# Kernel optimization log

Measured on AMD Instinct MI355X. Metric: run time of the kernel, lower is better.

The kernel has to match this reference:

```python
import jax, jax.numpy as jnp
import numpy as np

EOS = 1e-10
ALPHA = 0.5
TEMPERATURE = 1.0
BIAS = 0.0001
N_NODES = 8192
N_EDGES = 262144
INPUT_DIM = 512
HIDDEN = 128


def setup_inputs() -> dict:
    key = jax.random.key(0)
    ks = jax.random.split(key, 7)
    features = jax.random.normal(ks[0], (N_NODES, INPUT_DIM), dtype=jnp.float32)
    W_emb = jax.random.normal(ks[1], (HIDDEN, INPUT_DIM), dtype=jnp.float32) * (1.0 / np.sqrt(INPUT_DIM))
    b_emb = jax.random.normal(ks[2], (HIDDEN,), dtype=jnp.float32) * 0.01
    W_edge = jax.random.normal(ks[3], (1, 2 * HIDDEN), dtype=jnp.float32) * (1.0 / np.sqrt(2 * HIDDEN))
    b_edge = jax.random.normal(ks[4], (1,), dtype=jnp.float32) * 0.01
    noise = jax.random.uniform(ks[5], (N_EDGES,), dtype=jnp.float32)
    edges = jax.random.randint(ks[6], (2, N_EDGES), 0, N_NODES, dtype=jnp.int64 if jax.config.jax_enable_x64 else jnp.int32)
    return {"features": features, "W_emb": W_emb, "b_emb": b_emb,
            "W_edge": W_edge, "b_edge": b_edge, "noise": noise, "edges": edges}


def _sym_normalize(adj):
    # inv_sqrt_degree[:,None] * adj * inv_sqrt_degree[None,:]
    inv_sqrt_deg = 1.0 / (jnp.sqrt(adj.sum(axis=1)) + EOS)
    return adj * inv_sqrt_deg[:, None] * inv_sqrt_deg[None, :]


def reference(features, W_emb, b_emb, W_edge, b_edge, noise, edges):
    n = N_NODES
    # node embedding: single Linear + ReLU
    h = jax.nn.relu(features @ W_emb.T + b_emb)            # [N, H]
    e0, e1 = edges[0], edges[1]
    h0, h1 = h[e0], h[e1]                                   # [E, H] gathers
    Wa, Wb = W_edge[0, :HIDDEN], W_edge[0, HIDDEN:]
    s1 = h0 @ Wa + h1 @ Wb + b_edge[0]                       # edge_mlp(cat(h0,h1))
    s2 = h1 @ Wa + h0 @ Wb + b_edge[0]                       # edge_mlp(cat(h1,h0))
    raw = 0.5 * (s1 + s2)                                    # [E]
    # gumbel gate: eps = (bias-(1-bias))*rand + (1-bias)
    eps = (BIAS - (1.0 - BIAS)) * noise + (1.0 - BIAS)
    gate = (jnp.log(eps) - jnp.log1p(-eps) + raw) / TEMPERATURE
    weights_lp = jax.nn.sigmoid(gate)                        # [E]
    weights_hp = 1.0 - weights_lp
    eye = jnp.eye(n, dtype=features.dtype)
    # scatter edge weights to dense adjacency (assignment semantics, like torch adj[e0,e1]=w)
    adj_lp = jnp.zeros((n, n), dtype=features.dtype).at[e0, e1].set(weights_lp) + eye
    adj_lp = _sym_normalize(adj_lp)
    adj_hp = jnp.zeros((n, n), dtype=features.dtype).at[e0, e1].set(weights_hp) + eye
    adj_hp = _sym_normalize(adj_hp)
    mask = jnp.zeros((n, n), dtype=features.dtype).at[e0, e1].set(1.0)
    adj_hp = eye - adj_hp * mask * ALPHA
    return (adj_lp, adj_hp, weights_lp, weights_hp)
```

## Files before the change

### kernel.cpp

```cpp
#include <hip/hip_runtime.h>
#include <cstdint>
#include <cstddef>

#define N_NODES 8192
#define N_EDGES 262144
#define INPUT_DIM 512
#define HIDDEN 128
#define ALPHA 0.5f
#define EOS 1e-10f

#define BK 32
#define BM 32

__global__ __launch_bounds__(512) void k1_g(
    const float* __restrict__ F, const float* __restrict__ W,
    const float* __restrict__ bemb, const float* __restrict__ Wedge,
    float* __restrict__ g)
{
    __shared__ float Fl[BK][BM];
    __shared__ float Wl[BK][HIDDEN];
    int tid = threadIdx.x;
    int tx = tid & 15;
    int ty = tid >> 4;
    int node0 = blockIdx.x * BM;

    float acc[8];
#pragma unroll
    for (int j = 0; j < 8; j++) acc[j] = 0.f;

    for (int d0 = 0; d0 < INPUT_DIM; d0 += BK) {
        if (tid < 256) {
            int r = tid >> 3, dd = (tid & 7) << 2;
            float4 v = *(const float4*)&F[(size_t)(node0 + r) * INPUT_DIM + d0 + dd];
            Fl[dd + 0][r] = v.x; Fl[dd + 1][r] = v.y;
            Fl[dd + 2][r] = v.z; Fl[dd + 3][r] = v.w;
        }
#pragma unroll
        for (int i = 0; i < 2; i++) {
            int idx = tid + i * 512;
            int kr = idx >> 3, dd = (idx & 7) << 2;
            float4 v = *(const float4*)&W[(size_t)kr * INPUT_DIM + d0 + dd];
            Wl[dd + 0][kr] = v.x; Wl[dd + 1][kr] = v.y;
            Wl[dd + 2][kr] = v.z; Wl[dd + 3][kr] = v.w;
        }
        __syncthreads();
#pragma unroll
        for (int kk = 0; kk < BK; kk++) {
            float f0 = Fl[kk][ty];
            float4 wA = *(float4*)&Wl[kk][tx * 8];
            float4 wB = *(float4*)&Wl[kk][tx * 8 + 4];
            acc[0] = fmaf(f0, wA.x, acc[0]);
            acc[1] = fmaf(f0, wA.y, acc[1]);
            acc[2] = fmaf(f0, wA.z, acc[2]);
            acc[3] = fmaf(f0, wA.w, acc[3]);
            acc[4] = fmaf(f0, wB.x, acc[4]);
            acc[5] = fmaf(f0, wB.y, acc[5]);
            acc[6] = fmaf(f0, wB.z, acc[6]);
            acc[7] = fmaf(f0, wB.w, acc[7]);
        }
        __syncthreads();
    }
    float s = 0.f;
#pragma unroll
    for (int j = 0; j < 8; j++) {
        int k = tx * 8 + j;
        float h = acc[j] + bemb[k];
        h = h > 0.f ? h : 0.f;
        s += h * (Wedge[k] + Wedge[HIDDEN + k]);
    }
#pragma unroll
    for (int off = 8; off > 0; off >>= 1)
        s += __shfl_down(s, off, 16);
    if (tx == 0) g[node0 + ty] = s;
}

__global__ __launch_bounds__(256) void k2_edges(
    const int* __restrict__ edges, const float* __restrict__ noise,
    const float* __restrict__ g, const float* __restrict__ bedge,
    float* __restrict__ wlp, float* __restrict__ whp, int* __restrict__ lp_int)
{
    int i = blockIdx.x * 256 + threadIdx.x;
    if (i >= N_EDGES) return;
    int e0 = edges[i], e1 = edges[N_EDGES + i];
    float raw = 0.5f * (g[e0] + g[e1]) + bedge[0];
    const float c1 = (float)(0.0001 - (1.0 - 0.0001));
    const float c2 = (float)(1.0 - 0.0001);
    float eps = c1 * noise[i] + c2;
    float gate = logf(eps) - log1pf(-eps) + raw;
    float w = 1.f / (1.f + expf(-gate));
    wlp[i] = w;
    whp[i] = 1.f - w;
    atomicMax(&lp_int[(size_t)e0 * N_NODES + e1], i + 1);
}

__global__ __launch_bounds__(256) void k3_winner(
    const int* __restrict__ edges, const int* __restrict__ lp_int,
    const float* __restrict__ wlp, const float* __restrict__ whp,
    unsigned char* __restrict__ flags,
    float* __restrict__ deg_lp, float* __restrict__ deg_hp)
{
    int i = blockIdx.x * 256 + threadIdx.x;
    if (i >= N_EDGES) return;
    int e0 = edges[i], e1 = edges[N_EDGES + i];
    bool win = (lp_int[(size_t)e0 * N_NODES + e1] == i + 1);
    flags[i] = win ? 1 : 0;
    if (win) {
        atomicAdd(&deg_lp[e0], wlp[i]);
        atomicAdd(&deg_hp[e0], whp[i]);
    }
}

__global__ __launch_bounds__(256) void k4_inv(
    const float* __restrict__ deg_lp, const float* __restrict__ deg_hp,
    float* __restrict__ inv_lp, float* __restrict__ inv_hp)
{
    int r = blockIdx.x * 256 + threadIdx.x;
    if (r >= N_NODES) return;
    inv_lp[r] = 1.f / (sqrtf(deg_lp[r] + 1.f) + EOS);
    inv_hp[r] = 1.f / (sqrtf(deg_hp[r] + 1.f) + EOS);
}

__global__ __launch_bounds__(256) void k5_bg(
    float* __restrict__ LP, float* __restrict__ HP,
    const float* __restrict__ inv_lp)
{
    size_t idx = (size_t)blockIdx.x * 256 + threadIdx.x;
    int row = (int)(idx >> 11);
    int c4 = (int)(idx & 2047) << 2;
    float4 lp = make_float4(0.f, 0.f, 0.f, 0.f);
    float4 hp = make_float4(0.f, 0.f, 0.f, 0.f);
    int d = row - c4;
    if (d >= 0 && d < 4) {
        float il = inv_lp[row];
        ((float*)&lp)[d] = il * il;
        ((float*)&hp)[d] = 1.0f;
    }
    *(float4*)&LP[idx << 2] = lp;
    *(float4*)&HP[idx << 2] = hp;
}

__global__ __launch_bounds__(256) void k6_fix(
    const int* __restrict__ edges, const unsigned char* __restrict__ flags,
    const float* __restrict__ wlp, const float* __restrict__ whp,
    const float* __restrict__ inv_lp, const float* __restrict__ inv_hp,
    float* __restrict__ LP, float* __restrict__ HP)
{
    int i = blockIdx.x * 256 + threadIdx.x;
    if (i >= N_EDGES) return;
    if (!flags[i]) return;
    int r = edges[i], c = edges[N_EDGES + i];
    size_t cell = (size_t)r * N_NODES + c;
    float diag = (r == c) ? 1.f : 0.f;
    LP[cell] = (wlp[i] + diag) * inv_lp[r] * inv_lp[c];
    HP[cell] = diag - (whp[i] + diag) * inv_hp[r] * inv_hp[c] * ALPHA;
}

extern "C" void kernel_launch(void* const* d_in, const int* in_sizes, int n_in,
                              void* d_out, int out_size, void* d_ws, size_t ws_size,
                              hipStream_t stream) {
    const float* F     = (const float*)d_in[0];
    const float* W     = (const float*)d_in[1];
    const float* bemb  = (const float*)d_in[2];
    const float* Wedge = (const float*)d_in[3];
    const float* bedge = (const float*)d_in[4];
    const float* noise = (const float*)d_in[5];
    const int*   edges = (const int*)d_in[6];

    float* out = (float*)d_out;
    float* LP  = out;
    float* HP  = out + (size_t)N_NODES * N_NODES;
    float* wlp = HP + (size_t)N_NODES * N_NODES;
    float* whp = wlp + N_EDGES;

    char* ws = (char*)d_ws;
    float* g       = (float*)(ws);
    float* deg_lp  = (float*)(ws + 32768);
    float* deg_hp  = (float*)(ws + 65536);
    float* inv_lp  = (float*)(ws + 98304);
    float* inv_hp  = (float*)(ws + 131072);
    unsigned char* flags = (unsigned char*)(ws + 163840);

    hipMemsetAsync(deg_lp, 0, 2 * N_NODES * sizeof(float), stream);

    k1_g<<<N_NODES / BM, 512, 0, stream>>>(F, W, bemb, Wedge, g);
    k2_edges<<<N_EDGES / 256, 256, 0, stream>>>(edges, noise, g, bedge, wlp, whp, (int*)LP);
    k3_winner<<<N_EDGES / 256, 256, 0, stream>>>(edges, (const int*)LP, wlp, whp, flags, deg_lp, deg_hp);
    k4_inv<<<N_NODES / 256, 256, 0, stream>>>(deg_lp, deg_hp, inv_lp, inv_hp);
    k5_bg<<<(unsigned)(((size_t)N_NODES * N_NODES / 4) / 256), 256, 0, stream>>>(LP, HP, inv_lp);
    k6_fix<<<N_EDGES / 256, 256, 0, stream>>>(edges, flags, wlp, whp, inv_lp, inv_hp, LP, HP);
}
```

Baseline: 710.1 us.

## Track duplicate-edge losers in a list instead of a full winner pass

Each edge's weight is now added to the row degrees straight away in the edge kernel. The old value returned by atomicMax identifies duplicate (row, col) losers, which go into a small capped list; a later kernel subtracts their weights and flags them. This removes the separate winner kernel that re-read random dense-map cells for every edge. The dense-fill kernel is replaced by nontemporal vector zeroing of LP and HP, with the HP output used as the scatter map before it is zeroed, and diagonal entries are written in the inverse-degree kernel. Shared-memory padding is also added in the embedding GEMM; the cost is extra atomics per edge and a loser cap that could overflow with many duplicates.

```diff
diff --git a/kernel.cpp b/kernel.cpp
--- a/kernel.cpp
+++ b/kernel.cpp
@@ -8,17 +8,30 @@
 #define HIDDEN 128
 #define ALPHA 0.5f
 #define EOS 1e-10f
+#define LOSER_CAP 65536
 
 #define BK 32
 #define BM 32
+
+typedef float v4 __attribute__((ext_vector_type(4)));
+
+__global__ __launch_bounds__(256) void k_zero(v4* __restrict__ p)
+{
+    size_t base = (size_t)blockIdx.x * 2048 + threadIdx.x;
+#pragma unroll
+    for (int j = 0; j < 8; j++) {
+        v4 z = 0.f;
+        __builtin_nontemporal_store(z, &p[base + (size_t)j * 256]);
+    }
+}
 
 __global__ __launch_bounds__(512) void k1_g(
     const float* __restrict__ F, const float* __restrict__ W,
     const float* __restrict__ bemb, const float* __restrict__ Wedge,
     float* __restrict__ g)
 {
-    __shared__ float Fl[BK][BM];
-    __shared__ float Wl[BK][HIDDEN];
+    __shared__ float Fl[BK][BM + 1];
+    __shared__ float Wl[BK][HIDDEN + 4];
     int tid = threadIdx.x;
     int tx = tid & 15;
     int ty = tid >> 4;
@@ -77,66 +90,62 @@
 __global__ __launch_bounds__(256) void k2_edges(
     const int* __restrict__ edges, const float* __restrict__ noise,
     const float* __restrict__ g, const float* __restrict__ bedge,
-    float* __restrict__ wlp, float* __restrict__ whp, int* __restrict__ lp_int)
+    float* __restrict__ wlp, float* __restrict__ whp, int* __restrict__ map,
+    float* __restrict__ deg_lp, float* __restrict__ deg_hp,
+    int* __restrict__ loser_count, int* __restrict__ loser_list,
+    unsigned char* __restrict__ flags)
 {
     int i = blockIdx.x * 256 + threadIdx.x;
-    if (i >= N_EDGES) return;
     int e0 = edges[i], e1 = edges[N_EDGES + i];
     float raw = 0.5f * (g[e0] + g[e1]) + bedge[0];
-    const float c1 = (float)(0.0001 - (1.0 - 0.0001));
-    const float c2 = (float)(1.0 - 0.0001);
+    const float c1 = -0.9998f, c2 = 0.9999f;
     float eps = c1 * noise[i] + c2;
     float gate = logf(eps) - log1pf(-eps) + raw;
     float w = 1.f / (1.f + expf(-gate));
     wlp[i] = w;
     whp[i] = 1.f - w;
-    atomicMax(&lp_int[(size_t)e0 * N_NODES + e1], i + 1);
-}
-
-__global__ __launch_bounds__(256) void k3_winner(
-    const int* __restrict__ edges, const int* __restrict__ lp_int,
-    const float* __restrict__ wlp, const float* __restrict__ whp,
-    unsigned char* __restrict__ flags,
-    float* __restrict__ deg_lp, float* __restrict__ deg_hp)
-{
-    int i = blockIdx.x * 256 + threadIdx.x;
-    if (i >= N_EDGES) return;
-    int e0 = edges[i], e1 = edges[N_EDGES + i];
-    bool win = (lp_int[(size_t)e0 * N_NODES + e1] == i + 1);
-    flags[i] = win ? 1 : 0;
-    if (win) {
-        atomicAdd(&deg_lp[e0], wlp[i]);
-        atomicAdd(&deg_hp[e0], whp[i]);
-    }
-}
-
-__global__ __launch_bounds__(256) void k4_inv(
+    flags[i] = 0;
+    atomicAdd(&deg_lp[e0], w);
+    atomicAdd(&deg_hp[e0], 1.f - w);
+    int old = atomicMax(&map[(size_t)e0 * N_NODES + e1], i + 1);
+    if (old > 0) {
+        int loser = old < i + 1 ? old : i + 1;
+        int slot = atomicAdd(loser_count, 1);
+        if (slot < LOSER_CAP) loser_list[slot] = loser;
+    }
+}
+
+__global__ __launch_bounds__(256) void k3_losers(
+    const int* __restrict__ edges, const float* __restrict__ wlp,
+    const float* __restrict__ whp,
+    const int* __restrict__ loser_count, const int* __restrict__ loser_list,
+    float* __restrict__ deg_lp, float* __restrict__ deg_hp,
+    unsigned char* __restrict__ flags)
+{
+    int t = blockIdx.x * 256 + threadIdx.x;
+    int n = *loser_count;
+    if (n > LOSER_CAP) n = LOSER_CAP;
+    if (t >= n) return;
+    int i = loser_list[t] - 1;
+    int e0 = edges[i];
+    atomicAdd(&deg_lp[e0], -wlp[i]);
+    atomicAdd(&deg_hp[e0], -whp[i]);
+    flags[i] = 1;
+}
+
+__global__ __launch_bounds__(256) void k4_inv_diag(
     const float* __restrict__ deg_lp, const float* __restrict__ deg_hp,
-    float* __restrict__ inv_lp, float* __restrict__ inv_hp)
+    float* __restrict__ inv_lp, float* __restrict__ inv_hp,
+    float* __restrict__ LP, float* __restrict__ HP)
 {
     int r = blockIdx.x * 256 + threadIdx.x;
-    if (r >= N_NODES) return;
-    inv_lp[r] = 1.f / (sqrtf(deg_lp[r] + 1.f) + EOS);
-    inv_hp[r] = 1.f / (sqrtf(deg_hp[r] + 1.f) + EOS);
-}
-
-__global__ __launch_bounds__(256) void k5_bg(
-    float* __restrict__ LP, float* __restrict__ HP,
-    const float* __restrict__ inv_lp)
-{
-    size_t idx = (size_t)blockIdx.x * 256 + threadIdx.x;
-    int row = (int)(idx >> 11);
-    int c4 = (int)(idx & 2047) << 2;
-    float4 lp = make_float4(0.f, 0.f, 0.f, 0.f);
-    float4 hp = make_float4(0.f, 0.f, 0.f, 0.f);
-    int d = row - c4;
-    if (d >= 0 && d < 4) {
-        float il = inv_lp[row];
-        ((float*)&lp)[d] = il * il;
-        ((float*)&hp)[d] = 1.0f;
-    }
-    *(float4*)&LP[idx << 2] = lp;
-    *(float4*)&HP[idx << 2] = hp;
+    float il = 1.f / (sqrtf(deg_lp[r] + 1.f) + EOS);
+    float ih = 1.f / (sqrtf(deg_hp[r] + 1.f) + EOS);
+    inv_lp[r] = il;
+    inv_hp[r] = ih;
+    size_t d = (size_t)r * N_NODES + r;
+    LP[d] = il * il;
+    HP[d] = 1.0f;
 }
 
 __global__ __launch_bounds__(256) void k6_fix(
@@ -146,8 +155,7 @@
     float* __restrict__ LP, float* __restrict__ HP)
 {
     int i = blockIdx.x * 256 + threadIdx.x;
-    if (i >= N_EDGES) return;
-    if (!flags[i]) return;
+    if (flags[i]) return;
     int r = edges[i], c = edges[N_EDGES + i];
     size_t cell = (size_t)r * N_NODES + c;
     float diag = (r == c) ? 1.f : 0.f;
@@ -166,26 +174,32 @@
     const float* noise = (const float*)d_in[5];
     const int*   edges = (const int*)d_in[6];
 
+    const size_t N2 = (size_t)N_NODES * N_NODES;
     float* out = (float*)d_out;
     float* LP  = out;
-    float* HP  = out + (size_t)N_NODES * N_NODES;
-    float* wlp = HP + (size_t)N_NODES * N_NODES;
+    float* HP  = out + N2;
+    float* wlp = HP + N2;
     float* whp = wlp + N_EDGES;
 
     char* ws = (char*)d_ws;
-    float* g       = (float*)(ws);
-    float* deg_lp  = (float*)(ws + 32768);
-    float* deg_hp  = (float*)(ws + 65536);
-    float* inv_lp  = (float*)(ws + 98304);
-    float* inv_hp  = (float*)(ws + 131072);
-    unsigned char* flags = (unsigned char*)(ws + 163840);
-
-    hipMemsetAsync(deg_lp, 0, 2 * N_NODES * sizeof(float), stream);
-
+    float* g           = (float*)(ws);
+    float* deg_lp      = (float*)(ws + 32768);
+    float* deg_hp      = (float*)(ws + 65536);
+    int*   loser_count = (int*)  (ws + 98304);
+    float* inv_lp      = (float*)(ws + 98432);
+    float* inv_hp      = (float*)(ws + 131200);
+    int*   loser_list  = (int*)  (ws + 163968);
+    unsigned char* flags = (unsigned char*)(ws + 163968 + LOSER_CAP * 4);
+
+    hipMemsetAsync(deg_lp, 0, 65536 + 128, stream);
+
+    k_zero<<<8192, 256, 0, stream>>>((v4*)LP);
     k1_g<<<N_NODES / BM, 512, 0, stream>>>(F, W, bemb, Wedge, g);
-    k2_edges<<<N_EDGES / 256, 256, 0, stream>>>(edges, noise, g, bedge, wlp, whp, (int*)LP);
-    k3_winner<<<N_EDGES / 256, 256, 0, stream>>>(edges, (const int*)LP, wlp, whp, flags, deg_lp, deg_hp);
-    k4_inv<<<N_NODES / 256, 256, 0, stream>>>(deg_lp, deg_hp, inv_lp, inv_hp);
-    k5_bg<<<(unsigned)(((size_t)N_NODES * N_NODES / 4) / 256), 256, 0, stream>>>(LP, HP, inv_lp);
+    k2_edges<<<N_EDGES / 256, 256, 0, stream>>>(edges, noise, g, bedge,
+        wlp, whp, (int*)HP, deg_lp, deg_hp, loser_count, loser_list, flags);
+    k3_losers<<<LOSER_CAP / 256, 256, 0, stream>>>(edges, wlp, whp,
+        loser_count, loser_list, deg_lp, deg_hp, flags);
+    k_zero<<<8192, 256, 0, stream>>>((v4*)HP);
+    k4_inv_diag<<<N_NODES / 256, 256, 0, stream>>>(deg_lp, deg_hp, inv_lp, inv_hp, LP, HP);
     k6_fix<<<N_EDGES / 256, 256, 0, stream>>>(edges, flags, wlp, whp, inv_lp, inv_hp, LP, HP);
 }
```

Measured after the change: 697.9 us. About the same (-1.7%).
